# Performance work log

Hardware: AMD Instinct MI355X
Metric: run time of the kernel (lower is better)

Reference implementation:

```python
import jax, jax.numpy as jnp
import numpy as np

H, W = 256, 256
FOCAL = 50.0
N = 512


def setup_inputs() -> dict:
    key = jax.random.key(0)
    k1, k2, k3, k4 = jax.random.split(key, 4)
    means3d = jax.random.normal(k1, (N, 3), dtype=jnp.float32)
    scales = jax.random.uniform(k2, (N, 3), dtype=jnp.float32)
    opacities = jax.random.uniform(k3, (N, 1), dtype=jnp.float32)
    colors = jax.random.uniform(k4, (N, 3), dtype=jnp.float32)
    return {"means3d": means3d, "scales": scales, "opacities": opacities, "colors": colors}


def reference(means3d, scales, opacities, colors):
    # pixel grid (matches torch.meshgrid(u, v, indexing='xy') -> [H, W])
    u = jnp.arange(W, dtype=jnp.float32) - W / 2
    v = jnp.arange(H, dtype=jnp.float32) - H / 2
    uu, vv = jnp.meshgrid(u, v, indexing='xy')  # each [H, W]

    z = jnp.clip(means3d[:, 2], 0.1)            # [N]
    proj_u = FOCAL * means3d[:, 0] / z
    proj_v = FOCAL * means3d[:, 1] / z
    sigma_u = jnp.clip(FOCAL * scales[:, 0] / z, 0.5)
    sigma_v = jnp.clip(FOCAL * scales[:, 1] / z, 0.5)

    du = uu[None, :, :] - proj_u[:, None, None]  # [N, H, W]
    dv = vv[None, :, :] - proj_v[:, None, None]
    gauss = jnp.exp(-0.5 * (du ** 2 / sigma_u[:, None, None] ** 2
                            + dv ** 2 / sigma_v[:, None, None] ** 2))

    # front-to-back depth sort
    order = jnp.argsort(z)
    gauss = gauss[order]
    sorted_opac = opacities[order]          # [N, 1]
    sorted_colors = colors[order]           # [N, 3]

    alpha = jnp.clip(gauss * sorted_opac[:, :, None], 0.0, 1.0)  # [N, H, W]

    # Sequential alpha compositing: contribution_i = alpha_i * prod_{j<i}(1 - alpha_j) * color_i
    # Exclusive cumulative product of transmittance along N (exact closed form of the loop).
    trans = jnp.cumprod(1.0 - alpha, axis=0)                       # inclusive
    T = jnp.concatenate([jnp.ones((1, H, W), alpha.dtype), trans[:-1]], axis=0)  # exclusive
    image = jnp.einsum('nhw,nc->hwc', alpha * T, sorted_colors)    # [H, W, 3]
    return image
```

## Files before the change

kernel.cpp:

```cpp
#include <hip/hip_runtime.h>

#define IMG_W 256
#define IMG_H 256
#define NG 512
#define NSEG 16
#define SEGLEN (NG / NSEG)
#define PXT 64
#define PPT 4
#define FOCAL 50.0f

__global__ __launch_bounds__(1024, 1) void fused_kernel(
    const float* __restrict__ means3d, const float* __restrict__ scales,
    const float* __restrict__ opac, const float* __restrict__ colors,
    float* __restrict__ out)
{
    __shared__ __align__(16) unsigned long long zkey[NG];
    __shared__ int rpart[NG];
    __shared__ float4 ga[NG];
    __shared__ float2 gb[NG];
    __shared__ float4 part[NSEG - 1][PXT][PPT];

    const int tid = threadIdx.x;
    const int i = tid & (NG - 1);

    float z = 0.0f, mx = 0.0f, my = 0.0f;
    if (tid < NG) {
        mx = means3d[3 * i];
        my = means3d[3 * i + 1];
        z  = fmaxf(means3d[3 * i + 2], 0.1f);
        zkey[i] = ((unsigned long long)__float_as_uint(z) << 32) | (unsigned)i;
    }
    __syncthreads();

    const unsigned long long mykey = zkey[i];
    int cnt = 0;
    {
        const ulonglong2* kp = (const ulonglong2*)zkey + ((tid >> 9) * (NG / 4));
        #pragma unroll 8
        for (int jj = 0; jj < NG / 4; ++jj) {
            const ulonglong2 kk = kp[jj];
            cnt += (kk.x < mykey);
            cnt += (kk.y < mykey);
        }
    }
    if (tid >= NG) rpart[i] = cnt;
    __syncthreads();

    if (tid < NG) {
        const float inv_z = 1.0f / z;
        const float pu = FOCAL * mx * inv_z;
        const float pv = FOCAL * my * inv_z;
        const float su = fmaxf(FOCAL * scales[3 * i] * inv_z, 0.5f);
        const float sv = fmaxf(FOCAL * scales[3 * i + 1] * inv_z, 0.5f);
        const float k = -0.5f * 1.44269504088896340736f;
        const float a = k / (su * su);
        const float b = k / (sv * sv);
        const float lop = __log2f(opac[i]);
        const float dv = (float)blockIdx.x - (float)(IMG_H / 2) - pv;
        const float c = fmaf(dv * dv, b, lop);
        const int rank = cnt + rpart[i];
        ga[rank] = make_float4(pu, a, c, colors[3 * i]);
        gb[rank] = make_float2(colors[3 * i + 1], colors[3 * i + 2]);
    }
    __syncthreads();

    const int p   = tid & (PXT - 1);
    const int seg = tid >> 6;

    float u[PPT];
    #pragma unroll
    for (int j = 0; j < PPT; ++j) u[j] = (float)(p + PXT * j) - (float)(IMG_W / 2);

    float T[PPT], ar[PPT], ag[PPT], ab[PPT];
    #pragma unroll
    for (int j = 0; j < PPT; ++j) { T[j] = 1.0f; ar[j] = 0.0f; ag[j] = 0.0f; ab[j] = 0.0f; }

    const int base = seg * SEGLEN;
    #pragma unroll 4
    for (int n = 0; n < SEGLEN; ++n) {
        const float4 pa = ga[base + n];
        const float2 pb = gb[base + n];
        #pragma unroll
        for (int j = 0; j < PPT; ++j) {
            const float du = u[j] - pa.x;
            const float e = fmaf(du * du, pa.y, pa.z);
            const float al = __builtin_amdgcn_exp2f(e);
            const float w = al * T[j];
            ar[j] = fmaf(w, pa.w, ar[j]);
            ag[j] = fmaf(w, pb.x, ag[j]);
            ab[j] = fmaf(w, pb.y, ab[j]);
            T[j] -= w;
        }
    }

    if (seg) {
        #pragma unroll
        for (int j = 0; j < PPT; ++j)
            part[seg - 1][p][j] = make_float4(ar[j], ag[j], ab[j], T[j]);
    }
    __syncthreads();

    if (seg == 0) {
        for (int s = 1; s < NSEG; ++s) {
            #pragma unroll
            for (int j = 0; j < PPT; ++j) {
                const float4 q = part[s - 1][p][j];
                ar[j] = fmaf(T[j], q.x, ar[j]);
                ag[j] = fmaf(T[j], q.y, ag[j]);
                ab[j] = fmaf(T[j], q.z, ab[j]);
                T[j] *= q.w;
            }
        }
        const int row = blockIdx.x;
        #pragma unroll
        for (int j = 0; j < PPT; ++j) {
            const int pid = row * IMG_W + p + PXT * j;
            out[3 * pid]     = ar[j];
            out[3 * pid + 1] = ag[j];
            out[3 * pid + 2] = ab[j];
        }
    }
}

extern "C" void kernel_launch(void* const* d_in, const int* in_sizes, int n_in,
                              void* d_out, int out_size, void* d_ws, size_t ws_size,
                              hipStream_t stream) {
    const float* means3d = (const float*)d_in[0];
    const float* scales  = (const float*)d_in[1];
    const float* opac    = (const float*)d_in[2];
    const float* colors  = (const float*)d_in[3];
    float* out = (float*)d_out;

    fused_kernel<<<IMG_H, 1024, 0, stream>>>(means3d, scales, opac, colors, out);
}
```

Before: 21.14 us.

## Cull off-row Gaussians by horizontal extent and parallelize segment merge

Computes, per Gaussian and row, the horizontal pixel range where its contribution exceeds 2^-32 and skips Gaussians whose range misses the image. The skip is uniform across the wave. The final merge of segment partials is spread over 256 threads, one pixel each, instead of 64 threads handling four pixels each. This adds an extra float4 of shared storage per Gaussian and a sqrt per Gaussian, and drops negligible contributions.

```diff
diff --git a/kernel.cpp b/kernel.cpp
--- a/kernel.cpp
+++ b/kernel.cpp
@@ -16,9 +16,9 @@
 {
     __shared__ __align__(16) unsigned long long zkey[NG];
     __shared__ int rpart[NG];
-    __shared__ float4 ga[NG];
-    __shared__ float2 gb[NG];
-    __shared__ float4 part[NSEG - 1][PXT][PPT];
+    __shared__ float4 g0[NG];
+    __shared__ float4 g1[NG];
+    __shared__ float4 part[NSEG][PPT][PXT];
 
     const int tid = threadIdx.x;
     const int i = tid & (NG - 1);
@@ -58,9 +58,16 @@
         const float lop = __log2f(opac[i]);
         const float dv = (float)blockIdx.x - (float)(IMG_H / 2) - pv;
         const float c = fmaf(dv * dv, b, lop);
+        float lo = 1e9f, hi = 1e9f;
+        const float r2 = (c + 32.0f) / (-a);
+        if (r2 > 0.0f) {
+            const float R = sqrtf(r2);
+            lo = pu - R;
+            hi = pu + R;
+        }
         const int rank = cnt + rpart[i];
-        ga[rank] = make_float4(pu, a, c, colors[3 * i]);
-        gb[rank] = make_float2(colors[3 * i + 1], colors[3 * i + 2]);
+        g0[rank] = make_float4(lo, hi, pu, a);
+        g1[rank] = make_float4(c, colors[3 * i], colors[3 * i + 1], colors[3 * i + 2]);
     }
     __syncthreads();
 
@@ -78,47 +85,43 @@
     const int base = seg * SEGLEN;
     #pragma unroll 4
     for (int n = 0; n < SEGLEN; ++n) {
-        const float4 pa = ga[base + n];
-        const float2 pb = gb[base + n];
+        const float4 q0 = g0[base + n];
+        if (q0.y < -128.0f || q0.x > 127.0f) continue;
+        const float4 q1 = g1[base + n];
         #pragma unroll
         for (int j = 0; j < PPT; ++j) {
-            const float du = u[j] - pa.x;
-            const float e = fmaf(du * du, pa.y, pa.z);
+            const float du = u[j] - q0.z;
+            const float e = fmaf(du * du, q0.w, q1.x);
             const float al = __builtin_amdgcn_exp2f(e);
             const float w = al * T[j];
-            ar[j] = fmaf(w, pa.w, ar[j]);
-            ag[j] = fmaf(w, pb.x, ag[j]);
-            ab[j] = fmaf(w, pb.y, ab[j]);
+            ar[j] = fmaf(w, q1.y, ar[j]);
+            ag[j] = fmaf(w, q1.z, ag[j]);
+            ab[j] = fmaf(w, q1.w, ab[j]);
             T[j] -= w;
         }
     }
 
-    if (seg) {
-        #pragma unroll
-        for (int j = 0; j < PPT; ++j)
-            part[seg - 1][p][j] = make_float4(ar[j], ag[j], ab[j], T[j]);
-    }
+    #pragma unroll
+    for (int j = 0; j < PPT; ++j)
+        part[seg][j][p] = make_float4(ar[j], ag[j], ab[j], T[j]);
     __syncthreads();
 
-    if (seg == 0) {
+    if (tid < PPT * PXT) {
+        const int w  = tid >> 6;
+        const int pp = tid & (PXT - 1);
+        float4 acc = part[0][w][pp];
+        #pragma unroll
         for (int s = 1; s < NSEG; ++s) {
-            #pragma unroll
-            for (int j = 0; j < PPT; ++j) {
-                const float4 q = part[s - 1][p][j];
-                ar[j] = fmaf(T[j], q.x, ar[j]);
-                ag[j] = fmaf(T[j], q.y, ag[j]);
-                ab[j] = fmaf(T[j], q.z, ab[j]);
-                T[j] *= q.w;
-            }
+            const float4 q = part[s][w][pp];
+            acc.x = fmaf(acc.w, q.x, acc.x);
+            acc.y = fmaf(acc.w, q.y, acc.y);
+            acc.z = fmaf(acc.w, q.z, acc.z);
+            acc.w *= q.w;
         }
-        const int row = blockIdx.x;
-        #pragma unroll
-        for (int j = 0; j < PPT; ++j) {
-            const int pid = row * IMG_W + p + PXT * j;
-            out[3 * pid]     = ar[j];
-            out[3 * pid + 1] = ag[j];
-            out[3 * pid + 2] = ab[j];
-        }
+        const int pid = blockIdx.x * IMG_W + (w * PXT + pp);
+        out[3 * pid]     = acc.x;
+        out[3 * pid + 1] = acc.y;
+        out[3 * pid + 2] = acc.z;
     }
 }
 
```

New measurement: 20.76 us. Within noise of the previous version (-1.8%).
